# Kernel optimization log

Hardware: AMD Instinct MI355X
Metric: run time of the kernel (lower is better)

## Reference

```python
import jax, jax.numpy as jnp
import numpy as np

D = 768
H = 12
DH = D // H
PAIRS4 = [(0, 1), (0, 2), (0, 3), (1, 2), (1, 3), (2, 3)]
J6 = jnp.array([[0,0,0,0,0,1],[0,0,0,0,-1,0],[0,0,0,1,0,0],[0,0,1,0,0,0],[0,-1,0,0,0,0],[1,0,0,0,0,0]], dtype=jnp.float32)


def exterior(p1, p2):
    # p1,p2: (..., 4) -> normalized Plucker coords (..., 6)
    parts = [p1[..., i] * p2[..., j] - p1[..., j] * p2[..., i] for i, j in PAIRS4]
    L = jnp.stack(parts, axis=-1)
    n = jnp.clip(jnp.linalg.norm(L, axis=-1, keepdims=True), 1e-12)
    return L / n


def layernorm(x, g, b, eps=1e-5):
    m = jnp.mean(x, axis=-1, keepdims=True)
    v = jnp.var(x, axis=-1, keepdims=True)
    return (x - m) * jax.lax.rsqrt(v + eps) * g + b


def setup_inputs() -> dict:
    key = jax.random.key(0)
    ks = jax.random.split(key, 16)
    s = 0.02
    inp = {
        'x': jax.random.normal(ks[0], (1, 2048, D), dtype=jnp.float32),
        'ln1_g': jnp.ones((D,), jnp.float32), 'ln1_b': jnp.zeros((D,), jnp.float32),
        'qkv_w': jax.random.normal(ks[1], (D, 3 * D), jnp.float32) * s,
        'qkv_b': jnp.zeros((3 * D,), jnp.float32),
        'w1_write': jax.random.normal(ks[2], (D, 4 * H), jnp.float32) * s,
        'w2_write': jax.random.normal(ks[3], (D, 4 * H), jnp.float32) * s,
        'w1_read': jax.random.normal(ks[4], (D, 4 * H), jnp.float32) * s,
        'w2_read': jax.random.normal(ks[5], (D, 4 * H), jnp.float32) * s,
        'geo_v_w': jax.random.normal(ks[6], (D, D), jnp.float32) * s,
        'geo_v_b': jnp.zeros((D,), jnp.float32),
        'gate_w': jax.random.normal(ks[7], (D, H), jnp.float32) * s,
        'gate_b': jnp.zeros((H,), jnp.float32),
        'inc_scale': jnp.ones((H,), jnp.float32),
        'out_w': jax.random.normal(ks[8], (D, D), jnp.float32) * s,
        'out_b': jnp.zeros((D,), jnp.float32),
        'ln2_g': jnp.ones((D,), jnp.float32), 'ln2_b': jnp.zeros((D,), jnp.float32),
        'fc_w': jax.random.normal(ks[9], (D, 4 * D), jnp.float32) * s,
        'fc_b': jnp.zeros((4 * D,), jnp.float32),
        'proj_w': jax.random.normal(ks[10], (4 * D, D), jnp.float32) * s,
        'proj_b': jnp.zeros((D,), jnp.float32),
    }
    return inp


def dual_path_attention(x, qkv_w, qkv_b, w1_write, w2_write, w1_read, w2_read,
                        geo_v_w, geo_v_b, gate_w, gate_b, inc_scale, out_w, out_b):
    B, T, _ = x.shape
    scale = DH ** -0.5
    qkv = (x @ qkv_w + qkv_b).reshape(B, T, 3, H, DH)
    q = qkv[:, :, 0].transpose(0, 2, 1, 3)  # (B,H,T,dh)
    k = qkv[:, :, 1].transpose(0, 2, 1, 3)
    v = qkv[:, :, 2].transpose(0, 2, 1, 3)
    std_logits = jnp.einsum('bhtd,bhsd->bhts', q, k) * scale

    x_prev = jnp.concatenate([jnp.zeros((B, 1, x.shape[-1]), x.dtype), x[:, :-1]], axis=1)
    w1 = (x_prev @ w1_write).reshape(B, T, H, 4)
    w2 = (x @ w2_write).reshape(B, T, H, 4)
    write_lines = exterior(w1, w2)  # (B,T,H,6)
    r1 = (x @ w1_read).reshape(B, T, H, 4)
    r2 = (x @ w2_read).reshape(B, T, H, 4)
    read_lines = exterior(r1, r2)
    J_write = jnp.einsum('bthi,ij->bthj', write_lines, J6)
    geo_logits = jnp.einsum('bthp,bshp->bhts', read_lines, J_write)
    geo_logits = geo_logits * inc_scale[None, :, None, None]

    mask = jnp.triu(jnp.ones((T, T), dtype=bool), k=1)  # True above diagonal
    neg = jnp.finfo(x.dtype).min
    std_attn = jax.nn.softmax(jnp.where(mask, neg, std_logits), axis=-1)
    std_out = jnp.einsum('bhts,bhsd->bthd', std_attn, v).reshape(B, T, -1)
    geo_attn = jax.nn.softmax(jnp.where(mask, neg, geo_logits), axis=-1)
    geo_v = (x @ geo_v_w + geo_v_b).reshape(B, T, H, DH).transpose(0, 2, 1, 3)
    geo_out = jnp.einsum('bhts,bhsd->bthd', geo_attn, geo_v).reshape(B, T, -1)

    gate = jax.nn.sigmoid(x @ gate_w + gate_b).mean(axis=-1, keepdims=True)
    combined = (1 - gate) * std_out + gate * geo_out
    return combined @ out_w + out_b


def reference(x, ln1_g, ln1_b, qkv_w, qkv_b, w1_write, w2_write, w1_read, w2_read,
              geo_v_w, geo_v_b, gate_w, gate_b, inc_scale, out_w, out_b,
              ln2_g, ln2_b, fc_w, fc_b, proj_w, proj_b):
    h = x + dual_path_attention(layernorm(x, ln1_g, ln1_b), qkv_w, qkv_b,
                                w1_write, w2_write, w1_read, w2_read,
                                geo_v_w, geo_v_b, gate_w, gate_b, inc_scale,
                                out_w, out_b)
    m = layernorm(h, ln2_g, ln2_b)
    mlp = jax.nn.gelu(m @ fc_w + fc_b) @ proj_w + proj_b
    return h + mlp
```

## Files before the change

kernel.cpp:

```cpp
#include <hip/hip_runtime.h>
#include <hip/hip_bf16.h>
#include <math.h>

#define TT 2048
#define DD 768

typedef __bf16 bf16x8 __attribute__((ext_vector_type(8)));
typedef float f32x4 __attribute__((ext_vector_type(4)));

__device__ __forceinline__ void gload16(const void* g, void* l) {
    __builtin_amdgcn_global_load_lds(
        (const __attribute__((address_space(1))) unsigned int*)g,
        (__attribute__((address_space(3))) unsigned int*)l, 16, 0, 0);
}

__device__ __forceinline__ bf16x8 zero8() {
    bf16x8 v;
    #pragma unroll
    for (int j = 0; j < 8; ++j) v[j] = (__bf16)0.0f;
    return v;
}

__device__ __forceinline__ const __hip_bfloat16* opart_cptr(
    const __hip_bfloat16* pA, const __hip_bfloat16* pB, const __hip_bfloat16* pC, int slot)
{
    if (slot < 192) return pA + (size_t)slot * 8192;
    if (slot < 576) return pB + (size_t)(slot - 192) * 8192;
    return pC + (size_t)(slot - 576) * 8192;
}

__global__ __launch_bounds__(256) void ln_kernel(const float* __restrict__ in,
    const float* __restrict__ g, const float* __restrict__ b,
    __hip_bfloat16* __restrict__ out)
{
    const int t = blockIdx.x;
    const int tid = threadIdx.x;
    const float* row = in + (size_t)t * DD;
    float x0 = row[tid], x1 = row[tid + 256], x2 = row[tid + 512];
    float s = x0 + x1 + x2;
    float q = x0 * x0 + x1 * x1 + x2 * x2;
    #pragma unroll
    for (int m = 1; m < 64; m <<= 1) {
        s += __shfl_xor(s, m);
        q += __shfl_xor(q, m);
    }
    __shared__ float ssum[4], sqsum[4];
    const int w = tid >> 6;
    if ((tid & 63) == 0) { ssum[w] = s; sqsum[w] = q; }
    __syncthreads();
    s = ssum[0] + ssum[1] + ssum[2] + ssum[3];
    q = sqsum[0] + sqsum[1] + sqsum[2] + sqsum[3];
    const float mean = s * (1.0f / DD);
    const float var = q * (1.0f / DD) - mean * mean;
    const float rs = rsqrtf(var + 1e-5f);
    __hip_bfloat16* orow = out + (size_t)t * DD;
    orow[tid]       = __float2bfloat16((x0 - mean) * rs * g[tid]       + b[tid]);
    orow[tid + 256] = __float2bfloat16((x1 - mean) * rs * g[tid + 256] + b[tid + 256]);
    orow[tid + 512] = __float2bfloat16((x2 - mean) * rs * g[tid + 512] + b[tid + 512]);
}

__device__ __forceinline__ void castT_body(const float* __restrict__ in,
    __hip_bfloat16* __restrict__ out, int K, int N, int bx, int by, int tid,
    float (*tt)[33])
{
    const int n0 = bx << 5, k0 = by << 5;
    const int tx = tid & 31, ty = tid >> 5;
    #pragma unroll
    for (int i = 0; i < 32; i += 8)
        tt[ty + i][tx] = in[(size_t)(k0 + ty + i) * N + n0 + tx];
    __syncthreads();
    #pragma unroll
    for (int i = 0; i < 32; i += 8)
        out[(size_t)(n0 + ty + i) * K + k0 + tx] = __float2bfloat16(tt[tx][ty + i]);
}

__global__ __launch_bounds__(256) void prep_kernel(
    const float* __restrict__ w0, const float* __restrict__ w1, const float* __restrict__ w2,
    const float* __restrict__ w2w, const float* __restrict__ w1w,
    const float* __restrict__ w1r, const float* __restrict__ w2r,
    const float* __restrict__ gw, const float* __restrict__ qkv_b,
    const float* __restrict__ gvb,
    __hip_bfloat16* __restrict__ o0, __hip_bfloat16* __restrict__ o1,
    __hip_bfloat16* __restrict__ o2,
    __hip_bfloat16* __restrict__ Wcat, float* __restrict__ bias3, int mode)
{
    __shared__ float tt[32][33];
    const int bid = blockIdx.x;
    const int tid = threadIdx.x;
    if (mode == 0) {
        if (bid < 1728)      { castT_body(w0, o0, 768, 2304, bid % 72, bid / 72, tid, tt); return; }
        else if (bid < 2304) { int b = bid - 1728; castT_body(w1, o1, 768, 768, b % 24, b / 24, tid, tt); return; }
        const int wb = bid - 2304;
        if (wb >= 204) {
            const int idx = (wb - 204) * 256 + tid;
            float v = (idx < 2304) ? qkv_b[idx] : ((idx < 3072) ? gvb[idx - 2304] : 0.f);
            bias3[idx] = v;
            return;
        }
        const float* src; int col, stride;
        if (wb < 48)       { src = w2w; col = wb;       stride = 48; }
        else if (wb < 96)  { src = w1w; col = wb - 48;  stride = 48; }
        else if (wb < 144) { src = w1r; col = wb - 96;  stride = 48; }
        else if (wb < 192) { src = w2r; col = wb - 144; stride = 48; }
        else               { src = gw;  col = wb - 192; stride = 12; }
        #pragma unroll
        for (int i = 0; i < 3; ++i) {
            const int k = tid + (i << 8);
            Wcat[(size_t)wb * 768 + k] = __float2bfloat16(src[(size_t)k * stride + col]);
        }
    } else {
        if (bid < 576)       { castT_body(w0, o0, 768, 768, bid % 24, bid / 24, tid, tt); }
        else if (bid < 2880) { int b = bid - 576;  castT_body(w1, o1, 768, 3072, b % 96, b / 96, tid, tt); }
        else                 { int b = bid - 2880; castT_body(w2, o2, 3072, 768, b % 24, b / 24, tid, tt); }
    }
}

__device__ __forceinline__ float gelu_f(float x) {
    float u = 0.7978845608028654f * (x + 0.044715f * x * x * x);
    return 0.5f * x * (1.0f + tanhf(u));
}

__global__ __launch_bounds__(256) void mgemm_kernel(
    const __hip_bfloat16* __restrict__ A, const __hip_bfloat16* __restrict__ Bt,
    const float* __restrict__ bias, const float* __restrict__ resid,
    void* __restrict__ Cout, float* __restrict__ Pb0, float* __restrict__ Pb1,
    int M, int N, int K, int kz, int epi, int omode)
{
    __shared__ __hip_bfloat16 As[128 * 32];
    __shared__ __hip_bfloat16 Bs[64 * 32];
    const int tid = threadIdx.x;
    const int lane = tid & 63, w = tid >> 6;
    const int colBase = blockIdx.x << 6, rowBase = blockIdx.y << 7;
    const int z = blockIdx.z;
    const int Kc = K / kz, koff = z * Kc;

    const int lr = lane >> 2, pc = lane & 3;
    const int n = lane & 15, quad = lane >> 4;

    const int sr0 = (w << 4) + lr;
    const int sr1 = 64 + sr0;
    const int sc0 = (pc ^ ((sr0 >> 1) & 3)) << 3;

    f32x4 acc[2][4];
    #pragma unroll
    for (int i = 0; i < 2; ++i)
        #pragma unroll
        for (int j = 0; j < 4; ++j) acc[i][j] = (f32x4){0.f, 0.f, 0.f, 0.f};

    const int ar0 = (w << 5) + n;
    const int ar1 = ar0 + 16;
    const int ap0 = (quad ^ ((ar0 >> 1) & 3)) << 3;
    const int ap1 = (quad ^ ((ar1 >> 1) & 3)) << 3;

    for (int kk = koff; kk < koff + Kc; kk += 32) {
        __syncthreads();
        gload16(A  + (size_t)(rowBase + sr0) * K + kk + sc0, &As[(w << 4) * 32]);
        gload16(A  + (size_t)(rowBase + sr1) * K + kk + sc0, &As[(64 + (w << 4)) * 32]);
        gload16(Bt + (size_t)(colBase + sr0) * K + kk + sc0, &Bs[(w << 4) * 32]);
        __syncthreads();

        bf16x8 a0 = *(const bf16x8*)&As[ar0 * 32 + ap0];
        bf16x8 a1 = *(const bf16x8*)&As[ar1 * 32 + ap1];
        #pragma unroll
        for (int j = 0; j < 4; ++j) {
            const int rb = (j << 4) + n;
            bf16x8 bfj = *(const bf16x8*)&Bs[rb * 32 + ((quad ^ ((rb >> 1) & 3)) << 3)];
            acc[0][j] = __builtin_amdgcn_mfma_f32_16x16x32_bf16(a0, bfj, acc[0][j], 0, 0, 0);
            acc[1][j] = __builtin_amdgcn_mfma_f32_16x16x32_bf16(a1, bfj, acc[1][j], 0, 0, 0);
        }
    }

    if (kz == 1) {
        #pragma unroll
        for (int j = 0; j < 4; ++j) {
            const int col = colBase + (j << 4) + n;
            const float bj = bias ? bias[col] : 0.f;
            #pragma unroll
            for (int i = 0; i < 2; ++i) {
                #pragma unroll
                for (int r = 0; r < 4; ++r) {
                    const int row = rowBase + (w << 5) + (i << 4) + (quad << 2) + r;
                    float v = acc[i][j][r] + bj;
                    if (epi == 1) v = gelu_f(v);
                    else if (epi == 2) v += resid[(size_t)row * N + col];
                    if (omode == 1) ((__hip_bfloat16*)Cout)[(size_t)row * N + col] = __float2bfloat16(v);
                    else ((float*)Cout)[(size_t)row * N + col] = v;
                }
            }
        }
    } else {
        float* P = (z == 0) ? Pb0 : Pb1;
        #pragma unroll
        for (int j = 0; j < 4; ++j) {
            const int col = colBase + (j << 4) + n;
            #pragma unroll
            for (int i = 0; i < 2; ++i) {
                #pragma unroll
                for (int r = 0; r < 4; ++r) {
                    const int row = rowBase + (w << 5) + (i << 4) + (quad << 2) + r;
                    P[(size_t)row * N + col] = acc[i][j][r];
                }
            }
        }
    }
}

__global__ __launch_bounds__(256) void kred_kernel(
    const float* __restrict__ p0, const float* __restrict__ p1,
    const float* __restrict__ bias, const float* __restrict__ resid,
    float* __restrict__ out, int N)
{
    const int base = (blockIdx.x * 256 + threadIdx.x) << 2;
    float4 a = *(const float4*)&p0[base];
    float4 b = *(const float4*)&p1[base];
    float4 bi = *(const float4*)&bias[base % N];
    float4 rs = *(const float4*)&resid[base];
    float4 o;
    o.x = a.x + b.x + bi.x + rs.x;
    o.y = a.y + b.y + bi.y + rs.y;
    o.z = a.z + b.z + bi.z + rs.z;
    o.w = a.w + b.w + bi.w + rs.w;
    *(float4*)&out[base] = o;
}

__device__ __forceinline__ void exterior6(const float* a, const float* b, float* L) {
    L[0] = a[0] * b[1] - a[1] * b[0];
    L[1] = a[0] * b[2] - a[2] * b[0];
    L[2] = a[0] * b[3] - a[3] * b[0];
    L[3] = a[1] * b[2] - a[2] * b[1];
    L[4] = a[1] * b[3] - a[3] * b[1];
    L[5] = a[2] * b[3] - a[3] * b[2];
    float n = sqrtf(L[0]*L[0] + L[1]*L[1] + L[2]*L[2] + L[3]*L[3] + L[4]*L[4] + L[5]*L[5]);
    float inv = 1.f / fmaxf(n, 1e-12f);
    #pragma unroll
    for (int p = 0; p < 6; ++p) L[p] *= inv;
}

__global__ __launch_bounds__(64) void extgate_kernel(
    const __hip_bfloat16* __restrict__ Pall, const float* __restrict__ gb,
    __hip_bfloat16* __restrict__ rlb, __hip_bfloat16* __restrict__ jwb,
    float* __restrict__ gate)
{
    const int t = blockIdx.x;
    const int tid = threadIdx.x;
    const __hip_bfloat16* row = Pall + (size_t)t * 3328 + 3072;
    if (tid < 12) {
        const int h = tid;
        float a[4], b[4], L[6];
        #pragma unroll
        for (int i = 0; i < 4; ++i) {
            a[i] = (t > 0) ? __bfloat162float(row[-3328 + 48 + h * 4 + i]) : 0.f;
            b[i] = __bfloat162float(row[h * 4 + i]);
        }
        exterior6(a, b, L);
        __hip_bfloat16* jwp = jwb + (size_t)h * 16384 + t * 8;
        jwp[0] = __float2bfloat16( L[5]); jwp[1] = __float2bfloat16(-L[4]);
        jwp[2] = __float2bfloat16( L[3]); jwp[3] = __float2bfloat16( L[2]);
        jwp[4] = __float2bfloat16(-L[1]); jwp[5] = __float2bfloat16( L[0]);
        jwp[6] = __float2bfloat16(0.f);   jwp[7] = __float2bfloat16(0.f);
        #pragma unroll
        for (int i = 0; i < 4; ++i) {
            a[i] = __bfloat162float(row[96 + h * 4 + i]);
            b[i] = __bfloat162float(row[144 + h * 4 + i]);
        }
        exterior6(a, b, L);
        __hip_bfloat16* rlp = rlb + (size_t)h * 16384 + t * 8;
        #pragma unroll
        for (int p = 0; p < 6; ++p) rlp[p] = __float2bfloat16(L[p]);
        rlp[6] = __float2bfloat16(0.f); rlp[7] = __float2bfloat16(0.f);
    }
    if (tid == 32) {
        float g = 0.f;
        #pragma unroll
        for (int i = 0; i < 12; ++i)
            g += 1.f / (1.f + __expf(-(__bfloat162float(row[192 + i]) + gb[i])));
        gate[t] = g * (1.f / 12.f);
    }
}

__global__ __launch_bounds__(256) void vt_kernel(
    const __hip_bfloat16* __restrict__ qkvAll,
    __hip_bfloat16* __restrict__ VT, __hip_bfloat16* __restrict__ GVT)
{
    __shared__ __hip_bfloat16 tile[64][72];
    const int s0 = blockIdx.x << 6, h = blockIdx.y;
    const bool isGV = (blockIdx.z != 0);
    const __hip_bfloat16* src = qkvAll + (isGV ? 2304 : 1536) + h * 64;
    __hip_bfloat16* dst = (isGV ? GVT : VT) + (size_t)h * 131072;
    const int tid = threadIdx.x;
    const int r = tid >> 2, c = (tid & 3) << 3;
    *(bf16x8*)&tile[r][c]      = *(const bf16x8*)&src[(size_t)(s0 + r) * 3328 + c];
    *(bf16x8*)&tile[r][c + 32] = *(const bf16x8*)&src[(size_t)(s0 + r) * 3328 + c + 32];
    __syncthreads();
    __hip_bfloat16 tmp[8];
    #pragma unroll
    for (int j = 0; j < 8; ++j) tmp[j] = tile[c + j][r];
    *(bf16x8*)&dst[(size_t)r * 2048 + s0 + c] = *(const bf16x8*)tmp;
    #pragma unroll
    for (int j = 0; j < 8; ++j) tmp[j] = tile[c + 32 + j][r];
    *(bf16x8*)&dst[(size_t)r * 2048 + s0 + c + 32] = *(const bf16x8*)tmp;
}

__global__ __launch_bounds__(256) void mattn_kernel(
    const __hip_bfloat16* __restrict__ qkvAll, const __hip_bfloat16* __restrict__ VT,
    const __hip_bfloat16* __restrict__ GVT, const __hip_bfloat16* __restrict__ rlb,
    const __hip_bfloat16* __restrict__ jwb, const float* __restrict__ gate,
    const float* __restrict__ inc_scale, __hip_bfloat16* __restrict__ comb,
    __hip_bfloat16* __restrict__ OpA, __hip_bfloat16* __restrict__ OpB,
    __hip_bfloat16* __restrict__ OpC, float* __restrict__ stats)
{
    __shared__ __hip_bfloat16 Ks0[2048], Ks1[2048];
    __shared__ __hip_bfloat16 VTs0[2048], VTs1[2048];
    __shared__ __hip_bfloat16 GVTs0[2048], GVTs1[2048];
    __shared__ __hip_bfloat16 JWs[64][8];
    __shared__ __bf16 Ps[64][72];

    const int j = blockIdx.x;
    const int hh = blockIdx.y;
    int qt = 0, acc = 0, nc = 1;
    #pragma unroll 1
    for (;;) {
        nc = (qt + 9) / 9;
        if (j < acc + nc) break;
        acc += nc; ++qt;
    }
    const int c = j - acc;
    const int q0 = qt << 6;
    const int nk = qt + 1;
    const int ktb = c * nk / nc;
    const int kte = (c + 1) * nk / nc - 1;
    const int tid = threadIdx.x;
    const int w = tid >> 6, lane = tid & 63;
    const int n = lane & 15, quad = lane >> 4;

    const int qrow = q0 + (w << 4) + n;
    const size_t qb = (size_t)qrow * 3328 + hh * 64;
    bf16x8 af0 = *(const bf16x8*)&qkvAll[qb + (quad << 3)];
    bf16x8 af1 = *(const bf16x8*)&qkvAll[qb + 32 + (quad << 3)];
    bf16x8 rlA = zero8();
    if (quad == 0) rlA = *(const bf16x8*)&rlb[(size_t)hh * 16384 + (size_t)qrow * 8];
    const float isc = inc_scale[hh];
    const float mgc = fabsf(isc);
    const size_t vbase = (size_t)hh * 131072;

    const int sRow = tid >> 2, sc = tid & 3;
    const int sPos = ((sc ^ ((sRow >> 1) & 3)) << 3);
    const int sOff = sc << 3;

    f32x4 Os[4], Og[4];
    float m_s[4], lsp[4], lgp[4];
    #pragma unroll
    for (int r = 0; r < 4; ++r) {
        m_s[r] = -1e30f; lsp[r] = 0.f; lgp[r] = 0.f;
        Os[r] = (f32x4){0.f, 0.f, 0.f, 0.f};
        Og[r] = (f32x4){0.f, 0.f, 0.f, 0.f};
    }

    bf16x8 rK0, rK1, rV0, rV1, rG0, rG1, rJ = zero8();
    {
        const int k0 = ktb << 6;
        const size_t kb = (size_t)(k0 + sRow) * 3328 + 768 + hh * 64;
        const size_t vb = vbase + (size_t)sRow * 2048 + k0;
        rK0 = *(const bf16x8*)&qkvAll[kb + sOff];
        rK1 = *(const bf16x8*)&qkvAll[kb + sOff + 32];
        rV0 = *(const bf16x8*)&VT[vb + sOff];
        rV1 = *(const bf16x8*)&VT[vb + sOff + 32];
        rG0 = *(const bf16x8*)&GVT[vb + sOff];
        rG1 = *(const bf16x8*)&GVT[vb + sOff + 32];
        if (tid < 64) rJ = *(const bf16x8*)&jwb[(size_t)hh * 16384 + (size_t)(k0 + tid) * 8];
    }

    for (int kt = ktb; kt <= kte; ++kt) {
        const int k0 = kt << 6;
        __syncthreads();
        *(bf16x8*)&Ks0[sRow * 32 + sPos]  = rK0;
        *(bf16x8*)&Ks1[sRow * 32 + sPos]  = rK1;
        *(bf16x8*)&VTs0[sRow * 32 + sPos] = rV0;
        *(bf16x8*)&VTs1[sRow * 32 + sPos] = rV1;
        *(bf16x8*)&GVTs0[sRow * 32 + sPos] = rG0;
        *(bf16x8*)&GVTs1[sRow * 32 + sPos] = rG1;
        if (tid < 64) *(bf16x8*)&JWs[tid][0] = rJ;
        if (kt < kte) {
            const int k1 = (kt + 1) << 6;
            const size_t kb = (size_t)(k1 + sRow) * 3328 + 768 + hh * 64;
            const size_t vb = vbase + (size_t)sRow * 2048 + k1;
            rK0 = *(const bf16x8*)&qkvAll[kb + sOff];
            rK1 = *(const bf16x8*)&qkvAll[kb + sOff + 32];
            rV0 = *(const bf16x8*)&VT[vb + sOff];
            rV1 = *(const bf16x8*)&VT[vb + sOff + 32];
            rG0 = *(const bf16x8*)&GVT[vb + sOff];
            rG1 = *(const bf16x8*)&GVT[vb + sOff + 32];
            if (tid < 64) rJ = *(const bf16x8*)&jwb[(size_t)hh * 16384 + (size_t)(k1 + tid) * 8];
        }
        __syncthreads();

        f32x4 Ss[4], Sg[4];
        #pragma unroll
        for (int t = 0; t < 4; ++t) {
            Ss[t] = (f32x4){0.f, 0.f, 0.f, 0.f};
            Sg[t] = (f32x4){0.f, 0.f, 0.f, 0.f};
        }
        #pragma unroll
        for (int t = 0; t < 4; ++t) {
            const int krow = (t << 4) + n;
            const int kpos = ((quad ^ ((krow >> 1) & 3)) << 3);
            bf16x8 kb0 = *(const bf16x8*)&Ks0[krow * 32 + kpos];
            bf16x8 kb1 = *(const bf16x8*)&Ks1[krow * 32 + kpos];
            Ss[t] = __builtin_amdgcn_mfma_f32_16x16x32_bf16(af0, kb0, Ss[t], 0, 0, 0);
            Ss[t] = __builtin_amdgcn_mfma_f32_16x16x32_bf16(af1, kb1, Ss[t], 0, 0, 0);
            bf16x8 jb = zero8();
            if (quad == 0) jb = *(const bf16x8*)&JWs[krow][0];
            Sg[t] = __builtin_amdgcn_mfma_f32_16x16x32_bf16(rlA, jb, Sg[t], 0, 0, 0);
        }
        #pragma unroll
        for (int t = 0; t < 4; ++t) {
            #pragma unroll
            for (int r = 0; r < 4; ++r) { Ss[t][r] *= 0.125f; Sg[t][r] *= isc; }
        }
        if (kt == qt) {
            #pragma unroll
            for (int t = 0; t < 4; ++t) {
                const int sg = k0 + (t << 4) + n;
                #pragma unroll
                for (int r = 0; r < 4; ++r) {
                    const int qg = q0 + (w << 4) + (quad << 2) + r;
                    if (sg > qg) { Ss[t][r] = -1e30f; Sg[t][r] = -1e30f; }
                }
            }
        }

        #pragma unroll
        for (int r = 0; r < 4; ++r) {
            float mx = fmaxf(fmaxf(Ss[0][r], Ss[1][r]), fmaxf(Ss[2][r], Ss[3][r]));
            #pragma unroll
            for (int mk = 1; mk < 16; mk <<= 1) mx = fmaxf(mx, __shfl_xor(mx, mk));
            float mnew = fmaxf(m_s[r], mx);
            float alpha = __expf(m_s[r] - mnew);
            m_s[r] = mnew;
            float sm = 0.f;
            #pragma unroll
            for (int t = 0; t < 4; ++t) { Ss[t][r] = __expf(Ss[t][r] - mnew); sm += Ss[t][r]; }
            lsp[r] = lsp[r] * alpha + sm;
            #pragma unroll
            for (int t = 0; t < 4; ++t) Os[t][r] *= alpha;

            float smg = 0.f;
            #pragma unroll
            for (int t = 0; t < 4; ++t) { Sg[t][r] = __expf(Sg[t][r] - mgc); smg += Sg[t][r]; }
            lgp[r] += smg;
        }

        #pragma unroll
        for (int t = 0; t < 4; ++t) {
            #pragma unroll
            for (int r = 0; r < 4; ++r)
                Ps[(w << 4) + (quad << 2) + r][(t << 4) + n] = (__bf16)Ss[t][r];
        }
        asm volatile("s_waitcnt lgkmcnt(0)" ::: "memory");
        #pragma unroll
        for (int st = 0; st < 2; ++st) {
            bf16x8 ap = *(const bf16x8*)&Ps[(w << 4) + n][(st << 5) + (quad << 3)];
            const __hip_bfloat16* Vh = st ? VTs1 : VTs0;
            #pragma unroll
            for (int dt = 0; dt < 4; ++dt) {
                const int vrow = (dt << 4) + n;
                const int vpos = ((quad ^ ((vrow >> 1) & 3)) << 3);
                bf16x8 vb2 = *(const bf16x8*)&Vh[vrow * 32 + vpos];
                Os[dt] = __builtin_amdgcn_mfma_f32_16x16x32_bf16(ap, vb2, Os[dt], 0, 0, 0);
            }
        }
        asm volatile("s_waitcnt lgkmcnt(0)" ::: "memory");

        #pragma unroll
        for (int t = 0; t < 4; ++t) {
            #pragma unroll
            for (int r = 0; r < 4; ++r)
                Ps[(w << 4) + (quad << 2) + r][(t << 4) + n] = (__bf16)Sg[t][r];
        }
        asm volatile("s_waitcnt lgkmcnt(0)" ::: "memory");
        #pragma unroll
        for (int st = 0; st < 2; ++st) {
            bf16x8 gp = *(const bf16x8*)&Ps[(w << 4) + n][(st << 5) + (quad << 3)];
            const __hip_bfloat16* Gh = st ? GVTs1 : GVTs0;
            #pragma unroll
            for (int dt = 0; dt < 4; ++dt) {
                const int vrow = (dt << 4) + n;
                const int vpos = ((quad ^ ((vrow >> 1) & 3)) << 3);
                bf16x8 gb2 = *(const bf16x8*)&Gh[vrow * 32 + vpos];
                Og[dt] = __builtin_amdgcn_mfma_f32_16x16x32_bf16(gp, gb2, Og[dt], 0, 0, 0);
            }
        }
    }

    float l_s[4], l_g[4];
    #pragma unroll
    for (int r = 0; r < 4; ++r) {
        float ls = lsp[r], lg = lgp[r];
        #pragma unroll
        for (int mk = 1; mk < 16; mk <<= 1) {
            ls += __shfl_xor(ls, mk);
            lg += __shfl_xor(lg, mk);
        }
        l_s[r] = ls; l_g[r] = lg;
    }

    if (nc == 1) {
        #pragma unroll
        for (int r = 0; r < 4; ++r) {
            const int row = q0 + (w << 4) + (quad << 2) + r;
            const float g = gate[row];
            const float invs = (1.f - g) / l_s[r], invg = g / l_g[r];
            #pragma unroll
            for (int dt = 0; dt < 4; ++dt) {
                float val = Os[dt][r] * invs + Og[dt][r] * invg;
                comb[(size_t)row * DD + hh * 64 + (dt << 4) + n] = __float2bfloat16(val);
            }
        }
    } else {
        const int slot = hh * 74 + acc + c;
        __hip_bfloat16* op = (__hip_bfloat16*)opart_cptr(OpA, OpB, OpC, slot);
        float* st = stats + (size_t)slot * 256;
        #pragma unroll
        for (int r = 0; r < 4; ++r) {
            const int rloc = (w << 4) + (quad << 2) + r;
            #pragma unroll
            for (int dt = 0; dt < 4; ++dt) {
                const int col = (dt << 4) + n;
                op[rloc * 128 + col]      = __float2bfloat16(Os[dt][r]);
                op[rloc * 128 + 64 + col] = __float2bfloat16(Og[dt][r]);
            }
            if (n == 0) {
                st[rloc * 4 + 0] = m_s[r]; st[rloc * 4 + 1] = l_s[r];
                st[rloc * 4 + 2] = mgc;    st[rloc * 4 + 3] = l_g[r];
            }
        }
    }
}

__global__ __launch_bounds__(256) void acomb_kernel(
    const __hip_bfloat16* __restrict__ OpA, const __hip_bfloat16* __restrict__ OpB,
    const __hip_bfloat16* __restrict__ OpC, const float* __restrict__ stats,
    const float* __restrict__ gate, __hip_bfloat16* __restrict__ comb)
{
    const int qt = 9 + blockIdx.x;
    const int h = blockIdx.y;
    const int nc = (qt + 9) / 9;
    int acc = 0;
    #pragma unroll 1
    for (int q = 0; q < qt; ++q) acc += (q + 9) / 9;
    const int sb = h * 74 + acc;
    const int tid = threadIdx.x;
    const int rloc = tid >> 2;
    const int cseg = (tid & 3) << 4;
    const int row = (qt << 6) + rloc;
    float ms = -1e30f, mg = -1e30f;
    for (int c = 0; c < nc; ++c) {
        const float* st = stats + (size_t)(sb + c) * 256 + rloc * 4;
        ms = fmaxf(ms, st[0]);
        mg = fmaxf(mg, st[2]);
    }
    float wsc[4], wgc[4];
    float ls = 0.f, lg = 0.f;
    for (int c = 0; c < nc; ++c) {
        const float* st = stats + (size_t)(sb + c) * 256 + rloc * 4;
        wsc[c] = __expf(st[0] - ms); ls += st[1] * wsc[c];
        wgc[c] = __expf(st[2] - mg); lg += st[3] * wgc[c];
    }
    const float g = gate[row];
    const float fs = (1.f - g) / ls, fg = g / lg;
    #pragma unroll
    for (int cc = 0; cc < 16; ++cc) {
        const int col = cseg + cc;
        float os = 0.f, og = 0.f;
        for (int c = 0; c < nc; ++c) {
            const __hip_bfloat16* op = opart_cptr(OpA, OpB, OpC, sb + c) + rloc * 128;
            os += __bfloat162float(op[col]) * wsc[c];
            og += __bfloat162float(op[64 + col]) * wgc[c];
        }
        comb[(size_t)row * DD + h * 64 + col] = __float2bfloat16(os * fs + og * fg);
    }
}

extern "C" void kernel_launch(void* const* d_in, const int* in_sizes, int n_in,
                              void* d_out, int out_size, void* d_ws, size_t ws_size,
                              hipStream_t stream) {
    (void)in_sizes; (void)n_in; (void)out_size; (void)ws_size;
    const float* x      = (const float*)d_in[0];
    const float* ln1_g  = (const float*)d_in[1];
    const float* ln1_b  = (const float*)d_in[2];
    const float* qkv_w  = (const float*)d_in[3];
    const float* qkv_b  = (const float*)d_in[4];
    const float* w1w    = (const float*)d_in[5];
    const float* w2w    = (const float*)d_in[6];
    const float* w1r    = (const float*)d_in[7];
    const float* w2r    = (const float*)d_in[8];
    const float* gvw    = (const float*)d_in[9];
    const float* gvb    = (const float*)d_in[10];
    const float* gw     = (const float*)d_in[11];
    const float* gb     = (const float*)d_in[12];
    const float* isc    = (const float*)d_in[13];
    const float* ow     = (const float*)d_in[14];
    const float* ob     = (const float*)d_in[15];
    const float* ln2_g  = (const float*)d_in[16];
    const float* ln2_b  = (const float*)d_in[17];
    const float* fcw    = (const float*)d_in[18];
    const float* fcb    = (const float*)d_in[19];
    const float* pw     = (const float*)d_in[20];
    const float* pb     = (const float*)d_in[21];
    float* out = (float*)d_out;
    char* wsb  = (char*)d_ws;

    __hip_bfloat16* qkvAll = (__hip_bfloat16*)(wsb + 0);
    __hip_bfloat16* VTb    = (__hip_bfloat16*)(wsb + 13631488);
    __hip_bfloat16* GVTb   = (__hip_bfloat16*)(wsb + 16777216);
    __hip_bfloat16* rlb    = (__hip_bfloat16*)(wsb + 19922944);
    __hip_bfloat16* jwb    = (__hip_bfloat16*)(wsb + 20316160);
    float*          gate   = (float*)(wsb + 20709376);
    __hip_bfloat16* ln1    = (__hip_bfloat16*)(wsb + 20717568);
    __hip_bfloat16* comb   = (__hip_bfloat16*)(wsb + 23863296);
    float*          hbuf   = (float*)(wsb + 27009024);
    __hip_bfloat16* Bt     = (__hip_bfloat16*)(wsb + 33300480);
    float*          bias3  = (float*)(wsb + 38412288);
    __hip_bfloat16* owt    = (__hip_bfloat16*)(wsb + 38425600);

    __hip_bfloat16* OpA   = ln1;
    __hip_bfloat16* OpB   = (__hip_bfloat16*)hbuf;
    __hip_bfloat16* OpC   = Bt;
    float*          stats = (float*)owt;

    __hip_bfloat16* fcact  = qkvAll;
    __hip_bfloat16* pwt    = VTb;
    __hip_bfloat16* fcwt   = Bt;
    float* Ppart0 = (float*)(wsb + 20717568);
    float* Ppart1 = (float*)(wsb + 33300480);

    prep_kernel<<<2521, 256, 0, stream>>>(qkv_w, gvw, nullptr,
                                          w2w, w1w, w1r, w2r, gw, qkv_b, gvb,
                                          Bt, Bt + (size_t)2304 * 768, nullptr,
                                          Bt + (size_t)3072 * 768, bias3, 0);
    ln_kernel<<<TT, 256, 0, stream>>>(x, ln1_g, ln1_b, ln1);
    mgemm_kernel<<<dim3(52, 16, 1), 256, 0, stream>>>(ln1, Bt, bias3, nullptr, qkvAll,
                                                      nullptr, nullptr, TT, 3328, 768, 1, 0, 1);
    extgate_kernel<<<TT, 64, 0, stream>>>(qkvAll, gb, rlb, jwb, gate);
    vt_kernel<<<dim3(32, 12, 2), 256, 0, stream>>>(qkvAll, VTb, GVTb);
    mattn_kernel<<<dim3(74, 12), 256, 0, stream>>>(qkvAll, VTb, GVTb, rlb, jwb, gate, isc,
                                                   comb, OpA, OpB, OpC, stats);
    acomb_kernel<<<dim3(23, 12), 256, 0, stream>>>(OpA, OpB, OpC, stats, gate, comb);
    prep_kernel<<<5184, 256, 0, stream>>>(ow, fcw, pw,
                                          nullptr, nullptr, nullptr, nullptr,
                                          nullptr, nullptr, nullptr,
                                          owt, fcwt, pwt, nullptr, nullptr, 1);
    mgemm_kernel<<<dim3(12, 16, 1), 256, 0, stream>>>(comb, owt, ob, x, hbuf,
                                                      nullptr, nullptr, TT, 768, 768, 1, 2, 0);
    ln_kernel<<<TT, 256, 0, stream>>>(hbuf, ln2_g, ln2_b, ln1);
    mgemm_kernel<<<dim3(48, 16, 1), 256, 0, stream>>>(ln1, fcwt, fcb, nullptr, fcact,
                                                      nullptr, nullptr, TT, 3072, 768, 1, 1, 1);
    mgemm_kernel<<<dim3(12, 16, 2), 256, 0, stream>>>(fcact, pwt, pb, nullptr, nullptr,
                                                      Ppart0, Ppart1, TT, 768, 3072, 2, 0, 0);
    kred_kernel<<<1536, 256, 0, stream>>>(Ppart0, Ppart1, pb, hbuf, out, 768);
}
```

Before: 337.2 us.

## Fuse LN1 with weight prep, merge extgate with V transpose, rebalance attention split

Merges the first layernorm into the weight cast/transpose prep kernel and folds the exterior/gate kernel into the V-transpose kernel, cutting two launches. It changes the split-KV partitioning of attention from chunks of 9 to chunks of 8 query tiles, altering the grid to 80x12 and acomb to 24 blocks. Softmax switches to exp2f with the scale pre-multiplied by log2(e). The risk lies in the slot-indexing arithmetic and workspace sizing under the new partition.

```diff
diff --git a/kernel.cpp b/kernel.cpp
--- a/kernel.cpp
+++ b/kernel.cpp
@@ -29,12 +29,11 @@
     return pC + (size_t)(slot - 576) * 8192;
 }
 
-__global__ __launch_bounds__(256) void ln_kernel(const float* __restrict__ in,
+__device__ __forceinline__ void ln_body(const float* __restrict__ in,
     const float* __restrict__ g, const float* __restrict__ b,
-    __hip_bfloat16* __restrict__ out)
-{
-    const int t = blockIdx.x;
-    const int tid = threadIdx.x;
+    __hip_bfloat16* __restrict__ out, int t, int tid,
+    float* ssum, float* sqsum)
+{
     const float* row = in + (size_t)t * DD;
     float x0 = row[tid], x1 = row[tid + 256], x2 = row[tid + 512];
     float s = x0 + x1 + x2;
@@ -44,7 +43,6 @@
         s += __shfl_xor(s, m);
         q += __shfl_xor(q, m);
     }
-    __shared__ float ssum[4], sqsum[4];
     const int w = tid >> 6;
     if ((tid & 63) == 0) { ssum[w] = s; sqsum[w] = q; }
     __syncthreads();
@@ -59,6 +57,14 @@
     orow[tid + 512] = __float2bfloat16((x2 - mean) * rs * g[tid + 512] + b[tid + 512]);
 }
 
+__global__ __launch_bounds__(256) void ln_kernel(const float* __restrict__ in,
+    const float* __restrict__ g, const float* __restrict__ b,
+    __hip_bfloat16* __restrict__ out)
+{
+    __shared__ float ssum[4], sqsum[4];
+    ln_body(in, g, b, out, blockIdx.x, threadIdx.x, ssum, sqsum);
+}
+
 __device__ __forceinline__ void castT_body(const float* __restrict__ in,
     __hip_bfloat16* __restrict__ out, int K, int N, int bx, int by, int tid,
     float (*tt)[33])
@@ -74,45 +80,54 @@
         out[(size_t)(n0 + ty + i) * K + k0 + tx] = __float2bfloat16(tt[tx][ty + i]);
 }
 
-__global__ __launch_bounds__(256) void prep_kernel(
-    const float* __restrict__ w0, const float* __restrict__ w1, const float* __restrict__ w2,
+__global__ __launch_bounds__(256) void fused0_kernel(
+    const float* __restrict__ x, const float* __restrict__ ln1_g, const float* __restrict__ ln1_b,
+    __hip_bfloat16* __restrict__ ln1,
+    const float* __restrict__ qkv_w, const float* __restrict__ gvw,
     const float* __restrict__ w2w, const float* __restrict__ w1w,
     const float* __restrict__ w1r, const float* __restrict__ w2r,
     const float* __restrict__ gw, const float* __restrict__ qkv_b,
     const float* __restrict__ gvb,
-    __hip_bfloat16* __restrict__ o0, __hip_bfloat16* __restrict__ o1,
-    __hip_bfloat16* __restrict__ o2,
-    __hip_bfloat16* __restrict__ Wcat, float* __restrict__ bias3, int mode)
+    __hip_bfloat16* __restrict__ Bt, float* __restrict__ bias3)
 {
     __shared__ float tt[32][33];
     const int bid = blockIdx.x;
     const int tid = threadIdx.x;
-    if (mode == 0) {
-        if (bid < 1728)      { castT_body(w0, o0, 768, 2304, bid % 72, bid / 72, tid, tt); return; }
-        else if (bid < 2304) { int b = bid - 1728; castT_body(w1, o1, 768, 768, b % 24, b / 24, tid, tt); return; }
-        const int wb = bid - 2304;
-        if (wb >= 204) {
-            const int idx = (wb - 204) * 256 + tid;
-            float v = (idx < 2304) ? qkv_b[idx] : ((idx < 3072) ? gvb[idx - 2304] : 0.f);
-            bias3[idx] = v;
-            return;
-        }
-        const float* src; int col, stride;
-        if (wb < 48)       { src = w2w; col = wb;       stride = 48; }
-        else if (wb < 96)  { src = w1w; col = wb - 48;  stride = 48; }
-        else if (wb < 144) { src = w1r; col = wb - 96;  stride = 48; }
-        else if (wb < 192) { src = w2r; col = wb - 144; stride = 48; }
-        else               { src = gw;  col = wb - 192; stride = 12; }
-        #pragma unroll
-        for (int i = 0; i < 3; ++i) {
-            const int k = tid + (i << 8);
-            Wcat[(size_t)wb * 768 + k] = __float2bfloat16(src[(size_t)k * stride + col]);
-        }
-    } else {
-        if (bid < 576)       { castT_body(w0, o0, 768, 768, bid % 24, bid / 24, tid, tt); }
-        else if (bid < 2880) { int b = bid - 576;  castT_body(w1, o1, 768, 3072, b % 96, b / 96, tid, tt); }
-        else                 { int b = bid - 2880; castT_body(w2, o2, 3072, 768, b % 24, b / 24, tid, tt); }
-    }
+    if (bid < 2048) { ln_body(x, ln1_g, ln1_b, ln1, bid, tid, (float*)&tt[0][0], (float*)&tt[1][0]); return; }
+    const int pb = bid - 2048;
+    if (pb < 1728)      { castT_body(qkv_w, Bt, 768, 2304, pb % 72, pb / 72, tid, tt); return; }
+    else if (pb < 2304) { int b = pb - 1728; castT_body(gvw, Bt + (size_t)2304 * 768, 768, 768, b % 24, b / 24, tid, tt); return; }
+    const int wb = pb - 2304;
+    if (wb >= 204) {
+        const int idx = (wb - 204) * 256 + tid;
+        float v = (idx < 2304) ? qkv_b[idx] : ((idx < 3072) ? gvb[idx - 2304] : 0.f);
+        bias3[idx] = v;
+        return;
+    }
+    const float* src; int col, stride;
+    if (wb < 48)       { src = w2w; col = wb;       stride = 48; }
+    else if (wb < 96)  { src = w1w; col = wb - 48;  stride = 48; }
+    else if (wb < 144) { src = w1r; col = wb - 96;  stride = 48; }
+    else if (wb < 192) { src = w2r; col = wb - 144; stride = 48; }
+    else               { src = gw;  col = wb - 192; stride = 12; }
+    #pragma unroll
+    for (int i = 0; i < 3; ++i) {
+        const int k = tid + (i << 8);
+        Bt[(size_t)(3072 + wb) * 768 + k] = __float2bfloat16(src[(size_t)k * stride + col]);
+    }
+}
+
+__global__ __launch_bounds__(256) void prep1_kernel(
+    const float* __restrict__ w0, const float* __restrict__ w1, const float* __restrict__ w2,
+    __hip_bfloat16* __restrict__ o0, __hip_bfloat16* __restrict__ o1,
+    __hip_bfloat16* __restrict__ o2)
+{
+    __shared__ float tt[32][33];
+    const int bid = blockIdx.x;
+    const int tid = threadIdx.x;
+    if (bid < 576)       { castT_body(w0, o0, 768, 768, bid % 24, bid / 24, tid, tt); }
+    else if (bid < 2880) { int b = bid - 576;  castT_body(w1, o1, 768, 3072, b % 96, b / 96, tid, tt); }
+    else                 { int b = bid - 2880; castT_body(w2, o2, 3072, 768, b % 24, b / 24, tid, tt); }
 }
 
 __device__ __forceinline__ float gelu_f(float x) {
@@ -236,58 +251,60 @@
     for (int p = 0; p < 6; ++p) L[p] *= inv;
 }
 
-__global__ __launch_bounds__(64) void extgate_kernel(
-    const __hip_bfloat16* __restrict__ Pall, const float* __restrict__ gb,
+__global__ __launch_bounds__(256) void fusedev_kernel(
+    const __hip_bfloat16* __restrict__ qkvAll, const float* __restrict__ gb,
     __hip_bfloat16* __restrict__ rlb, __hip_bfloat16* __restrict__ jwb,
-    float* __restrict__ gate)
-{
-    const int t = blockIdx.x;
+    float* __restrict__ gate,
+    __hip_bfloat16* __restrict__ VT, __hip_bfloat16* __restrict__ GVT)
+{
+    __shared__ __hip_bfloat16 tile[64][72];
+    const int bid = blockIdx.x;
     const int tid = threadIdx.x;
-    const __hip_bfloat16* row = Pall + (size_t)t * 3328 + 3072;
-    if (tid < 12) {
-        const int h = tid;
-        float a[4], b[4], L[6];
-        #pragma unroll
-        for (int i = 0; i < 4; ++i) {
-            a[i] = (t > 0) ? __bfloat162float(row[-3328 + 48 + h * 4 + i]) : 0.f;
-            b[i] = __bfloat162float(row[h * 4 + i]);
-        }
-        exterior6(a, b, L);
-        __hip_bfloat16* jwp = jwb + (size_t)h * 16384 + t * 8;
-        jwp[0] = __float2bfloat16( L[5]); jwp[1] = __float2bfloat16(-L[4]);
-        jwp[2] = __float2bfloat16( L[3]); jwp[3] = __float2bfloat16( L[2]);
-        jwp[4] = __float2bfloat16(-L[1]); jwp[5] = __float2bfloat16( L[0]);
-        jwp[6] = __float2bfloat16(0.f);   jwp[7] = __float2bfloat16(0.f);
-        #pragma unroll
-        for (int i = 0; i < 4; ++i) {
-            a[i] = __bfloat162float(row[96 + h * 4 + i]);
-            b[i] = __bfloat162float(row[144 + h * 4 + i]);
-        }
-        exterior6(a, b, L);
-        __hip_bfloat16* rlp = rlb + (size_t)h * 16384 + t * 8;
-        #pragma unroll
-        for (int p = 0; p < 6; ++p) rlp[p] = __float2bfloat16(L[p]);
-        rlp[6] = __float2bfloat16(0.f); rlp[7] = __float2bfloat16(0.f);
-    }
-    if (tid == 32) {
-        float g = 0.f;
-        #pragma unroll
-        for (int i = 0; i < 12; ++i)
-            g += 1.f / (1.f + __expf(-(__bfloat162float(row[192 + i]) + gb[i])));
-        gate[t] = g * (1.f / 12.f);
-    }
-}
-
-__global__ __launch_bounds__(256) void vt_kernel(
-    const __hip_bfloat16* __restrict__ qkvAll,
-    __hip_bfloat16* __restrict__ VT, __hip_bfloat16* __restrict__ GVT)
-{
-    __shared__ __hip_bfloat16 tile[64][72];
-    const int s0 = blockIdx.x << 6, h = blockIdx.y;
-    const bool isGV = (blockIdx.z != 0);
+    if (bid < 512) {
+        const int t = (bid << 2) | (tid >> 6);
+        const int lane = tid & 63;
+        const __hip_bfloat16* row = qkvAll + (size_t)t * 3328 + 3072;
+        if (lane < 12) {
+            const int h = lane;
+            float a[4], b[4], L[6];
+            #pragma unroll
+            for (int i = 0; i < 4; ++i) {
+                a[i] = (t > 0) ? __bfloat162float(row[-3328 + 48 + h * 4 + i]) : 0.f;
+                b[i] = __bfloat162float(row[h * 4 + i]);
+            }
+            exterior6(a, b, L);
+            __hip_bfloat16* jwp = jwb + (size_t)h * 16384 + t * 8;
+            jwp[0] = __float2bfloat16( L[5]); jwp[1] = __float2bfloat16(-L[4]);
+            jwp[2] = __float2bfloat16( L[3]); jwp[3] = __float2bfloat16( L[2]);
+            jwp[4] = __float2bfloat16(-L[1]); jwp[5] = __float2bfloat16( L[0]);
+            jwp[6] = __float2bfloat16(0.f);   jwp[7] = __float2bfloat16(0.f);
+            #pragma unroll
+            for (int i = 0; i < 4; ++i) {
+                a[i] = __bfloat162float(row[96 + h * 4 + i]);
+                b[i] = __bfloat162float(row[144 + h * 4 + i]);
+            }
+            exterior6(a, b, L);
+            __hip_bfloat16* rlp = rlb + (size_t)h * 16384 + t * 8;
+            #pragma unroll
+            for (int p = 0; p < 6; ++p) rlp[p] = __float2bfloat16(L[p]);
+            rlp[6] = __float2bfloat16(0.f); rlp[7] = __float2bfloat16(0.f);
+        }
+        if (lane == 32) {
+            float g = 0.f;
+            #pragma unroll
+            for (int i = 0; i < 12; ++i)
+                g += 1.f / (1.f + __expf(-(__bfloat162float(row[192 + i]) + gb[i])));
+            gate[t] = g * (1.f / 12.f);
+        }
+        return;
+    }
+    const int b = bid - 512;
+    const bool isGV = (b >= 384);
+    const int rem = isGV ? (b - 384) : b;
+    const int h = rem >> 5;
+    const int s0 = (rem & 31) << 6;
     const __hip_bfloat16* src = qkvAll + (isGV ? 2304 : 1536) + h * 64;
     __hip_bfloat16* dst = (isGV ? GVT : VT) + (size_t)h * 131072;
-    const int tid = threadIdx.x;
     const int r = tid >> 2, c = (tid & 3) << 3;
     *(bf16x8*)&tile[r][c]      = *(const bf16x8*)&src[(size_t)(s0 + r) * 3328 + c];
     *(bf16x8*)&tile[r][c + 32] = *(const bf16x8*)&src[(size_t)(s0 + r) * 3328 + c + 32];
@@ -320,7 +337,7 @@
     int qt = 0, acc = 0, nc = 1;
     #pragma unroll 1
     for (;;) {
-        nc = (qt + 9) / 9;
+        nc = (qt >> 3) + 1;
         if (j < acc + nc) break;
         acc += nc; ++qt;
     }
@@ -339,8 +356,9 @@
     bf16x8 af1 = *(const bf16x8*)&qkvAll[qb + 32 + (quad << 3)];
     bf16x8 rlA = zero8();
     if (quad == 0) rlA = *(const bf16x8*)&rlb[(size_t)hh * 16384 + (size_t)qrow * 8];
-    const float isc = inc_scale[hh];
-    const float mgc = fabsf(isc);
+    const float SCL = 0.18033688011112042f;
+    const float isc2 = inc_scale[hh] * 1.4426950408889634f;
+    const float mgc2 = fabsf(isc2);
     const size_t vbase = (size_t)hh * 131072;
 
     const int sRow = tid >> 2, sc = tid & 3;
@@ -415,7 +433,7 @@
         #pragma unroll
         for (int t = 0; t < 4; ++t) {
             #pragma unroll
-            for (int r = 0; r < 4; ++r) { Ss[t][r] *= 0.125f; Sg[t][r] *= isc; }
+            for (int r = 0; r < 4; ++r) { Ss[t][r] *= SCL; Sg[t][r] *= isc2; }
         }
         if (kt == qt) {
             #pragma unroll
@@ -435,18 +453,18 @@
             #pragma unroll
             for (int mk = 1; mk < 16; mk <<= 1) mx = fmaxf(mx, __shfl_xor(mx, mk));
             float mnew = fmaxf(m_s[r], mx);
-            float alpha = __expf(m_s[r] - mnew);
+            float alpha = exp2f(m_s[r] - mnew);
             m_s[r] = mnew;
             float sm = 0.f;
             #pragma unroll
-            for (int t = 0; t < 4; ++t) { Ss[t][r] = __expf(Ss[t][r] - mnew); sm += Ss[t][r]; }
+            for (int t = 0; t < 4; ++t) { Ss[t][r] = exp2f(Ss[t][r] - mnew); sm += Ss[t][r]; }
             lsp[r] = lsp[r] * alpha + sm;
             #pragma unroll
             for (int t = 0; t < 4; ++t) Os[t][r] *= alpha;
 
             float smg = 0.f;
             #pragma unroll
-            for (int t = 0; t < 4; ++t) { Sg[t][r] = __expf(Sg[t][r] - mgc); smg += Sg[t][r]; }
+            for (int t = 0; t < 4; ++t) { Sg[t][r] = exp2f(Sg[t][r] - mgc2); smg += Sg[t][r]; }
             lgp[r] += smg;
         }
 
@@ -517,7 +535,7 @@
             }
         }
     } else {
-        const int slot = hh * 74 + acc + c;
+        const int slot = hh * 72 + (acc - 8) + c;
         __hip_bfloat16* op = (__hip_bfloat16*)opart_cptr(OpA, OpB, OpC, slot);
         float* st = stats + (size_t)slot * 256;
         #pragma unroll
@@ -531,7 +549,7 @@
             }
             if (n == 0) {
                 st[rloc * 4 + 0] = m_s[r]; st[rloc * 4 + 1] = l_s[r];
-                st[rloc * 4 + 2] = mgc;    st[rloc * 4 + 3] = l_g[r];
+                st[rloc * 4 + 2] = mgc2;   st[rloc * 4 + 3] = l_g[r];
             }
         }
     }
@@ -542,13 +560,13 @@
     const __hip_bfloat16* __restrict__ OpC, const float* __restrict__ stats,
     const float* __restrict__ gate, __hip_bfloat16* __restrict__ comb)
 {
-    const int qt = 9 + blockIdx.x;
+    const int qt = 8 + blockIdx.x;
     const int h = blockIdx.y;
-    const int nc = (qt + 9) / 9;
+    const int nc = (qt >> 3) + 1;
     int acc = 0;
     #pragma unroll 1
-    for (int q = 0; q < qt; ++q) acc += (q + 9) / 9;
-    const int sb = h * 74 + acc;
+    for (int q = 0; q < qt; ++q) acc += (q >> 3) + 1;
+    const int sb = h * 72 + acc - 8;
     const int tid = threadIdx.x;
     const int rloc = tid >> 2;
     const int cseg = (tid & 3) << 4;
@@ -563,8 +581,8 @@
     float ls = 0.f, lg = 0.f;
     for (int c = 0; c < nc; ++c) {
         const float* st = stats + (size_t)(sb + c) * 256 + rloc * 4;
-        wsc[c] = __expf(st[0] - ms); ls += st[1] * wsc[c];
-        wgc[c] = __expf(st[2] - mg); lg += st[3] * wgc[c];
+        wsc[c] = exp2f(st[0] - ms); ls += st[1] * wsc[c];
+        wgc[c] = exp2f(st[2] - mg); lg += st[3] * wgc[c];
     }
     const float g = gate[row];
     const float fs = (1.f - g) / ls, fg = g / lg;
@@ -634,22 +652,16 @@
     float* Ppart0 = (float*)(wsb + 20717568);
     float* Ppart1 = (float*)(wsb + 33300480);
 
-    prep_kernel<<<2521, 256, 0, stream>>>(qkv_w, gvw, nullptr,
-                                          w2w, w1w, w1r, w2r, gw, qkv_b, gvb,
-                                          Bt, Bt + (size_t)2304 * 768, nullptr,
-                                          Bt + (size_t)3072 * 768, bias3, 0);
-    ln_kernel<<<TT, 256, 0, stream>>>(x, ln1_g, ln1_b, ln1);
+    fused0_kernel<<<4569, 256, 0, stream>>>(x, ln1_g, ln1_b, ln1,
+                                            qkv_w, gvw, w2w, w1w, w1r, w2r, gw, qkv_b, gvb,
+                                            Bt, bias3);
     mgemm_kernel<<<dim3(52, 16, 1), 256, 0, stream>>>(ln1, Bt, bias3, nullptr, qkvAll,
                                                       nullptr, nullptr, TT, 3328, 768, 1, 0, 1);
-    extgate_kernel<<<TT, 64, 0, stream>>>(qkvAll, gb, rlb, jwb, gate);
-    vt_kernel<<<dim3(32, 12, 2), 256, 0, stream>>>(qkvAll, VTb, GVTb);
-    mattn_kernel<<<dim3(74, 12), 256, 0, stream>>>(qkvAll, VTb, GVTb, rlb, jwb, gate, isc,
+    fusedev_kernel<<<1280, 256, 0, stream>>>(qkvAll, gb, rlb, jwb, gate, VTb, GVTb);
+    mattn_kernel<<<dim3(80, 12), 256, 0, stream>>>(qkvAll, VTb, GVTb, rlb, jwb, gate, isc,
                                                    comb, OpA, OpB, OpC, stats);
-    acomb_kernel<<<dim3(23, 12), 256, 0, stream>>>(OpA, OpB, OpC, stats, gate, comb);
-    prep_kernel<<<5184, 256, 0, stream>>>(ow, fcw, pw,
-                                          nullptr, nullptr, nullptr, nullptr,
-                                          nullptr, nullptr, nullptr,
-                                          owt, fcwt, pwt, nullptr, nullptr, 1);
+    acomb_kernel<<<dim3(24, 12), 256, 0, stream>>>(OpA, OpB, OpC, stats, gate, comb);
+    prep1_kernel<<<5184, 256, 0, stream>>>(ow, fcw, pw, owt, fcwt, pwt);
     mgemm_kernel<<<dim3(12, 16, 1), 256, 0, stream>>>(comb, owt, ob, x, hbuf,
                                                       nullptr, nullptr, TT, 768, 768, 1, 2, 0);
     ln_kernel<<<TT, 256, 0, stream>>>(hbuf, ln2_g, ln2_b, ln1);
```

After: 334.6 us. About the same (-0.8%).
